# Kernel tuning notes

Hardware: AMD Instinct MI355X
Metric: run time of the kernel (lower is better)

## Reference

```python
import jax, jax.numpy as jnp
import numpy as np

NUM_HEADS = 32
NUM_KV_HEADS = 8
HEAD_DIM = 128
ROPE_THETA = 10000.0
HIDDEN = NUM_HEADS * HEAD_DIM


def setup_inputs() -> dict:
    key = jax.random.key(0)
    ks = jax.random.split(key, 5)
    B, S = 2, 2048
    hidden_states = jax.random.normal(ks[0], (B, S, HIDDEN), dtype=jnp.float32)
    wq = jax.random.normal(ks[1], (HIDDEN, HIDDEN), dtype=jnp.float32) * 0.02
    wk = jax.random.normal(ks[2], (NUM_KV_HEADS * HEAD_DIM, HIDDEN), dtype=jnp.float32) * 0.02
    wv = jax.random.normal(ks[3], (NUM_KV_HEADS * HEAD_DIM, HIDDEN), dtype=jnp.float32) * 0.02
    wo = jax.random.normal(ks[4], (HIDDEN, HIDDEN), dtype=jnp.float32) * 0.02
    position_ids = jnp.broadcast_to(jnp.arange(S, dtype=jnp.int64 if jax.config.read('jax_enable_x64') else jnp.int32)[None, :], (B, S))
    return {"hidden_states": hidden_states, "position_ids": position_ids,
            "wq": wq, "wk": wk, "wv": wv, "wo": wo}


def _rotate_half(x):
    x1, x2 = jnp.split(x, 2, axis=-1)
    return jnp.concatenate((-x2, x1), axis=-1)


def _rope_tables(position_ids, dtype):
    # inv_freq: [head_dim/2]
    inv_freq = 1.0 / (ROPE_THETA ** (jnp.arange(0, HEAD_DIM, 2, dtype=jnp.float32) / HEAD_DIM))
    # freqs per position: [B, S, head_dim/2] -> emb [B, S, head_dim]
    freqs = position_ids.astype(jnp.float32)[..., None] * inv_freq  # bsd2
    emb = jnp.concatenate((freqs, freqs), axis=-1)
    # unsqueeze head dim -> [B, 1, S, head_dim]
    return jnp.cos(emb).astype(dtype)[:, None], jnp.sin(emb).astype(dtype)[:, None]


def reference(hidden_states, position_ids, wq, wk, wv, wo):
    B, S, H = hidden_states.shape
    n_rep = NUM_HEADS // NUM_KV_HEADS
    # projections (torch Linear: x @ W^T)
    q = (hidden_states @ wq.T).reshape(B, S, NUM_HEADS, HEAD_DIM).transpose(0, 2, 1, 3)
    k = (hidden_states @ wk.T).reshape(B, S, NUM_KV_HEADS, HEAD_DIM).transpose(0, 2, 1, 3)
    v = (hidden_states @ wv.T).reshape(B, S, NUM_KV_HEADS, HEAD_DIM).transpose(0, 2, 1, 3)
    cos, sin = _rope_tables(position_ids, hidden_states.dtype)
    q = q * cos + _rotate_half(q) * sin
    k = k * cos + _rotate_half(k) * sin
    # repeat_kv: [B, kvH, S, D] -> [B, H, S, D]
    k = jnp.repeat(k, n_rep, axis=1)
    v = jnp.repeat(v, n_rep, axis=1)
    scale = 1.0 / jnp.sqrt(jnp.asarray(HEAD_DIM, dtype=hidden_states.dtype))
    scores = jnp.einsum('bhqd,bhkd->bhqk', q, k) * scale
    causal = jnp.tril(jnp.ones((S, S), dtype=bool))
    scores = jnp.where(causal[None, None], scores, jnp.finfo(scores.dtype).min)
    # softmax in fp32 then cast back (matches HF upcast)
    attn = jax.nn.softmax(scores.astype(jnp.float32), axis=-1).astype(q.dtype)
    out = jnp.einsum('bhqk,bhkd->bhqd', attn, v)
    out = out.transpose(0, 2, 1, 3).reshape(B, S, H)
    return out @ wo.T
```

## Files before the change

### kernel.cpp

```cpp
#include <hip/hip_runtime.h>
#include <stdint.h>

#define NH      32
#define NKVH    8
#define HD      128
#define BATCH   2
#define SEQ     2048
#define HIDDEN  4096
#define KVDIM   1024
#define TOKENS  (BATCH*SEQ)

typedef __bf16 bf16x8 __attribute__((ext_vector_type(8)));
typedef float  f32x4  __attribute__((ext_vector_type(4)));

__device__ __forceinline__ uint16_t f32_to_bf16(float f) {
  union { float f; uint32_t u; } v; v.f = f;
  uint32_t r = v.u + 0x7FFFu + ((v.u >> 16) & 1u);
  return (uint16_t)(r >> 16);
}
__device__ __forceinline__ float bf16_to_f32(uint16_t h) {
  union { uint32_t u; float f; } v; v.u = ((uint32_t)h) << 16;
  return v.f;
}
__device__ __forceinline__ bf16x8 ld_frag(const uint16_t* p) {
  return *(const bf16x8*)p;
}
#define MFMA_BF16(a,b,c) __builtin_amdgcn_mfma_f32_16x16x32_bf16((a),(b),(c),0,0,0)
#define NEG_BIG (-1.0e30f)

typedef __attribute__((address_space(1))) void as1_void;
typedef __attribute__((address_space(3))) void as3_void;
__device__ __forceinline__ void gload_lds16(const void* g, void* l) {
  __builtin_amdgcn_global_load_lds((as1_void*)g, (as3_void*)l, 16, 0, 0);
}

__device__ __forceinline__ void cvt8(const float* __restrict__ s,
                                     uint16_t* __restrict__ d, size_t i) {
  const float4* sp = (const float4*)s + 2*i;
  float4 a = sp[0], b = sp[1];
  union { uint16_t u[8]; uint4 v; } o;
  o.u[0]=f32_to_bf16(a.x); o.u[1]=f32_to_bf16(a.y);
  o.u[2]=f32_to_bf16(a.z); o.u[3]=f32_to_bf16(a.w);
  o.u[4]=f32_to_bf16(b.x); o.u[5]=f32_to_bf16(b.y);
  o.u[6]=f32_to_bf16(b.z); o.u[7]=f32_to_bf16(b.w);
  ((uint4*)d)[i] = o.v;
}

__global__ __launch_bounds__(256) void cvt_all(
    const float* __restrict__ X,  const float* __restrict__ Wq,
    const float* __restrict__ Wk, const float* __restrict__ Wv,
    uint16_t* __restrict__ R0, uint16_t* __restrict__ R1,
    uint16_t* __restrict__ R2, uint16_t* __restrict__ R3)
{
  int blk = blockIdx.x;
  const float* s; uint16_t* d; int b0;
  if (blk < 8192)       { s = X;  d = R0; b0 = 0; }
  else if (blk < 16384) { s = Wq; d = R1; b0 = 8192; }
  else if (blk < 18432) { s = Wk; d = R2; b0 = 16384; }
  else                  { s = Wv; d = R3; b0 = 18432; }
  cvt8(s, d, (size_t)(blk - b0)*256 + threadIdx.x);
}

__global__ __launch_bounds__(256) void cvt_one(
    const float* __restrict__ s, uint16_t* __restrict__ d)
{
  cvt8(s, d, (size_t)blockIdx.x*256 + threadIdx.x);
}

__device__ __forceinline__ void store_c(uint16_t* p, float v) { *p = f32_to_bf16(v); }
__device__ __forceinline__ void store_c(float*    p, float v) { *p = v; }

template <typename TC>
__device__ __forceinline__ void gemm_body(
    const uint16_t* __restrict__ A, const uint16_t* __restrict__ B,
    TC* __restrict__ C, int m0, int n0, int N, int K)
{
  __shared__ __align__(16) uint16_t As[3][128*32];
  __shared__ __align__(16) uint16_t Bs[3][128*32];
  const int tid  = threadIdx.x;
  const int wave = tid >> 6;
  const int lane = tid & 63;
  const int wm = (wave >> 1) * 64;
  const int wn = (wave & 1) * 64;
  const int srow = lane >> 2;
  const int scol = (((lane & 3) ^ ((lane >> 3) & 3)) * 8);
  const uint16_t* Ap = A + (size_t)(m0 + wave*16 + srow) * K + scol;
  const uint16_t* Bp = B + (size_t)(n0 + wave*16 + srow) * K + scol;
  const int wuo = wave*16*32;
  const int fr = lane & 15;
  const int fo = (((lane >> 4) ^ ((fr >> 1) & 3)) * 8);
  const int NT = K / 32;

  #pragma unroll
  for (int t = 0; t < 2; ++t) {
    gload_lds16(Ap + (size_t)t*32,                &As[t][wuo]);
    gload_lds16(Ap + (size_t)64*K + (size_t)t*32, &As[t][64*32 + wuo]);
    gload_lds16(Bp + (size_t)t*32,                &Bs[t][wuo]);
    gload_lds16(Bp + (size_t)64*K + (size_t)t*32, &Bs[t][64*32 + wuo]);
  }

  f32x4 acc[4][4] = {};
  int s_cur = 0, s_stage = 2;
  for (int t = 0; t < NT; ++t) {
    if (t < NT - 1) asm volatile("s_waitcnt vmcnt(4)" ::: "memory");
    else            asm volatile("s_waitcnt vmcnt(0)" ::: "memory");
    __builtin_amdgcn_s_barrier();
    asm volatile("" ::: "memory");

    if (t + 2 < NT) {
      const size_t k2 = (size_t)(t + 2) * 32;
      gload_lds16(Ap + k2,                &As[s_stage][wuo]);
      gload_lds16(Ap + (size_t)64*K + k2, &As[s_stage][64*32 + wuo]);
      gload_lds16(Bp + k2,                &Bs[s_stage][wuo]);
      gload_lds16(Bp + (size_t)64*K + k2, &Bs[s_stage][64*32 + wuo]);
    }

    const uint16_t* Asb = As[s_cur];
    const uint16_t* Bsb = Bs[s_cur];
    bf16x8 af[4], bfr[4];
    #pragma unroll
    for (int i = 0; i < 4; ++i) af[i]  = ld_frag(&Asb[(wm + i*16 + fr)*32 + fo]);
    #pragma unroll
    for (int j = 0; j < 4; ++j) bfr[j] = ld_frag(&Bsb[(wn + j*16 + fr)*32 + fo]);
    __builtin_amdgcn_s_setprio(1);
    #pragma unroll
    for (int i = 0; i < 4; ++i)
      #pragma unroll
      for (int j = 0; j < 4; ++j)
        acc[i][j] = MFMA_BF16(af[i], bfr[j], acc[i][j]);
    __builtin_amdgcn_s_setprio(0);

    s_cur   = (s_cur   == 2) ? 0 : s_cur + 1;
    s_stage = (s_stage == 2) ? 0 : s_stage + 1;
  }

  const int cr = (lane >> 4) * 4;
  const int cfr = lane & 15;
  #pragma unroll
  for (int i = 0; i < 4; ++i)
    #pragma unroll
    for (int j = 0; j < 4; ++j)
      #pragma unroll
      for (int r = 0; r < 4; ++r)
        store_c(&C[(size_t)(m0 + wm + i*16 + cr + r) * N + (n0 + wn + j*16 + cfr)],
                acc[i][j][r]);
}

__global__ __launch_bounds__(256, 3) void qkv_gemm(
    const uint16_t* __restrict__ X,
    const uint16_t* __restrict__ Wq, const uint16_t* __restrict__ Wk,
    const uint16_t* __restrict__ Wv,
    uint16_t* __restrict__ Qo, uint16_t* __restrict__ Ko, uint16_t* __restrict__ Vo)
{
  int bx = blockIdx.x;
  const uint16_t* B; uint16_t* C; int n0, N;
  if (bx < 32)      { B = Wq; C = Qo; n0 = bx*128;      N = HIDDEN; }
  else if (bx < 40) { B = Wk; C = Ko; n0 = (bx-32)*128; N = KVDIM;  }
  else              { B = Wv; C = Vo; n0 = (bx-40)*128; N = KVDIM;  }
  gemm_body<uint16_t>(X, B, C, blockIdx.y*128, n0, N, HIDDEN);
}

__global__ __launch_bounds__(256, 3) void out_gemm(
    const uint16_t* __restrict__ A, const uint16_t* __restrict__ B,
    float* __restrict__ C, int N, int K)
{
  gemm_body<float>(A, B, C, blockIdx.y*128, blockIdx.x*128, N, K);
}

__global__ __launch_bounds__(256) void rope_kernel(
    uint16_t* __restrict__ Q, uint16_t* __restrict__ K)
{
  int idx = blockIdx.x * 256 + threadIdx.x;
  int j = idx & 63;
  int rest = idx >> 6;
  int h = rest % (NH + NKVH);
  int t = rest / (NH + NKVH);
  float pos = (float)(t % SEQ);
  float inv_freq = __exp10f(-0.0625f * (float)j);
  float ang = pos * inv_freq;
  float s, c;
  __sincosf(ang, &s, &c);
  uint16_t* base = (h < NH) ? (Q + (size_t)t*HIDDEN + h*HD)
                            : (K + (size_t)t*KVDIM + (h-NH)*HD);
  float x1 = bf16_to_f32(base[j]);
  float x2 = bf16_to_f32(base[j+64]);
  base[j]    = f32_to_bf16(x1*c - x2*s);
  base[j+64] = f32_to_bf16(x2*c + x1*s);
}

__global__ __launch_bounds__(256) void transpose_v(
    const uint16_t* __restrict__ V, uint16_t* __restrict__ Vt)
{
  __shared__ uint16_t tile[64][66];
  int bh = blockIdx.z;  int b = bh >> 3, h = bh & 7;
  int s0 = blockIdx.x * 64;
  int d0 = blockIdx.y * 64;
  int tx = threadIdx.x & 63;
  int ty = threadIdx.x >> 6;
  const uint16_t* Vp = V + (size_t)b*SEQ*KVDIM + (size_t)h*HD;
  for (int r = ty; r < 64; r += 4)
    tile[r][tx] = Vp[(size_t)(s0 + r)*KVDIM + d0 + tx];
  __syncthreads();
  uint16_t* Vtp = Vt + ((size_t)b*NKVH + h)*HD*SEQ;
  for (int r = ty; r < 64; r += 4)
    Vtp[(size_t)(d0 + r)*SEQ + s0 + tx] = tile[tx][r];
}

#define KSTR 136
#define VSTR 72

__global__ __launch_bounds__(256, 4) void flash_attn(
    uint16_t* __restrict__ Q, const uint16_t* __restrict__ K,
    const uint16_t* __restrict__ Vt)
{
  __shared__ __align__(16) uint16_t Ks[64*KSTR];
  __shared__ __align__(16) uint16_t Vs[128*VSTR];
  uint16_t* Ps = Ks;

  const int tid  = threadIdx.x;
  const int wave = tid >> 6;
  const int lane = tid & 63;
  const int fr = lane & 15;
  const int g  = lane >> 4;
  const int fo = g * 8;
  const int bh = blockIdx.y;
  const int b = bh >> 5, h = bh & 31;
  const int kvh = h >> 2;

  uint16_t*       Qh = Q  + (size_t)b*SEQ*HIDDEN + (size_t)h*HD;
  const uint16_t* Kp = K  + (size_t)b*SEQ*KVDIM  + (size_t)kvh*HD;
  const uint16_t* Vp = Vt + ((size_t)b*NKVH + kvh)*HD*SEQ;

  #pragma unroll
  for (int pass = 0; pass < 2; ++pass) {
    const int qt = pass ? (31 - (int)blockIdx.x) : (int)blockIdx.x;
    const int q0 = qt * 64;
    const int qrow_base = q0 + wave*16 + g*4;

    bf16x8 qf[4];
    #pragma unroll
    for (int ks = 0; ks < 4; ++ks)
      qf[ks] = ld_frag(Qh + (size_t)(q0 + wave*16 + fr)*HIDDEN + ks*32 + fo);

    float m_i[4], l_i[4];
    f32x4 oacc[8] = {};
    #pragma unroll
    for (int r = 0; r < 4; ++r) { m_i[r] = NEG_BIG; l_i[r] = 0.f; }

    const int nkt = qt + 1;
    for (int kt = 0; kt < nkt; ++kt) {
      const int k0 = kt * 64;
      __syncthreads();
      #pragma unroll
      for (int i = 0; i < 4; ++i) {
        int gi = tid + i*256;
        int kr = gi >> 4, kc = (gi & 15) * 8;
        *(bf16x8*)&Ks[kr*KSTR + kc] = *(const bf16x8*)(Kp + (size_t)(k0 + kr)*KVDIM + kc);
        int vr = gi >> 3, vc = (gi & 7) * 8;
        *(bf16x8*)&Vs[vr*VSTR + vc] = *(const bf16x8*)(Vp + (size_t)vr*SEQ + k0 + vc);
      }
      __syncthreads();

      f32x4 sacc[4] = {};
      #pragma unroll
      for (int ks = 0; ks < 4; ++ks) {
        bf16x8 bk[4];
        #pragma unroll
        for (int j = 0; j < 4; ++j) bk[j] = ld_frag(&Ks[(j*16 + fr)*KSTR + ks*32 + fo]);
        #pragma unroll
        for (int j = 0; j < 4; ++j) sacc[j] = MFMA_BF16(qf[ks], bk[j], sacc[j]);
      }

      const bool diag = (kt == qt);
      #pragma unroll
      for (int r = 0; r < 4; ++r) {
        float vals[4];
        #pragma unroll
        for (int j = 0; j < 4; ++j) {
          float v = sacc[j][r] * 0.08838834764831845f;
          if (diag && (k0 + j*16 + fr > qrow_base + r)) v = NEG_BIG;
          vals[j] = v;
        }
        float mt = fmaxf(fmaxf(vals[0], vals[1]), fmaxf(vals[2], vals[3]));
        #pragma unroll
        for (int off = 1; off < 16; off <<= 1) mt = fmaxf(mt, __shfl_xor(mt, off, 64));
        float mn = fmaxf(m_i[r], mt);
        float alpha = __expf(fminf(m_i[r] - mn, 0.f));
        float lt = 0.f;
        #pragma unroll
        for (int j = 0; j < 4; ++j) {
          float p = __expf(fminf(vals[j] - mn, 0.f));
          sacc[j][r] = p;
          lt += p;
        }
        #pragma unroll
        for (int off = 1; off < 16; off <<= 1) lt += __shfl_xor(lt, off, 64);
        m_i[r] = mn;
        l_i[r] = l_i[r]*alpha + lt;
        #pragma unroll
        for (int n = 0; n < 8; ++n) oacc[n][r] *= alpha;
      }

      __syncthreads();

      #pragma unroll
      for (int j = 0; j < 4; ++j)
        #pragma unroll
        for (int r = 0; r < 4; ++r)
          Ps[(wave*16 + g*4 + r)*VSTR + j*16 + fr] = f32_to_bf16(sacc[j][r]);

      #pragma unroll
      for (int ks = 0; ks < 2; ++ks) {
        bf16x8 ap = ld_frag(&Ps[(wave*16 + fr)*VSTR + ks*32 + fo]);
        #pragma unroll
        for (int half = 0; half < 2; ++half) {
          bf16x8 bv[4];
          #pragma unroll
          for (int n = 0; n < 4; ++n)
            bv[n] = ld_frag(&Vs[((half*4 + n)*16 + fr)*VSTR + ks*32 + fo]);
          #pragma unroll
          for (int n = 0; n < 4; ++n)
            oacc[half*4 + n] = MFMA_BF16(ap, bv[n], oacc[half*4 + n]);
        }
      }
    }

    #pragma unroll
    for (int r = 0; r < 4; ++r) {
      float inv_l = 1.0f / l_i[r];
      #pragma unroll
      for (int n = 0; n < 8; ++n)
        Qh[(size_t)(qrow_base + r)*HIDDEN + n*16 + fr] = f32_to_bf16(oacc[n][r] * inv_l);
    }
    __syncthreads();
  }
}

extern "C" void kernel_launch(void* const* d_in, const int* in_sizes, int n_in,
                              void* d_out, int out_size, void* d_ws, size_t ws_size,
                              hipStream_t stream)
{
  (void)in_sizes; (void)n_in; (void)out_size; (void)ws_size;
  const float* hidden = (const float*)d_in[0];
  const float* wq = (const float*)d_in[2];
  const float* wk = (const float*)d_in[3];
  const float* wv = (const float*)d_in[4];
  const float* wo = (const float*)d_in[5];
  float* out = (float*)d_out;

  uint16_t* R0 = (uint16_t*)d_ws;
  uint16_t* R1 = R0 + (size_t)HIDDEN*HIDDEN;
  uint16_t* R2 = R1 + (size_t)HIDDEN*HIDDEN;
  uint16_t* R3 = R2 + (size_t)KVDIM*HIDDEN;
  uint16_t* Qb = R3 + (size_t)KVDIM*HIDDEN;
  uint16_t* Kb = Qb + (size_t)TOKENS*HIDDEN;
  uint16_t* Vb = Kb + (size_t)TOKENS*KVDIM;

  dim3 blk(256);
  cvt_all<<<dim3(20480), blk, 0, stream>>>(hidden, wq, wk, wv, R0, R1, R2, R3);
  qkv_gemm<<<dim3(48, TOKENS/128), blk, 0, stream>>>(R0, R1, R2, R3, Qb, Kb, Vb);
  rope_kernel<<<dim3(TOKENS*(NH+NKVH)*64/256), blk, 0, stream>>>(Qb, Kb);
  cvt_one<<<dim3(HIDDEN*HIDDEN/8/256), blk, 0, stream>>>(wo, R0);
  transpose_v<<<dim3(SEQ/64, HD/64, BATCH*NKVH), blk, 0, stream>>>(Vb, R1);
  flash_attn<<<dim3(16, BATCH*NH), blk, 0, stream>>>(Qb, Kb, R1);
  out_gemm<<<dim3(HIDDEN/128, TOKENS/128), blk, 0, stream>>>(Qb, R0, out, HIDDEN, HIDDEN);
}
```

Baseline: 840.5 us.

## Transpose QK^T MFMA layout and add lazy softmax rescaling

Swaps the MFMA operands so each lane holds a full query row's scores. This lets the row max and sum use two cross-lane shuffles instead of four per row, and the probabilities are written to LDS as packed 8-byte stores. It adds a lazy-rescale threshold that skips the alpha rescale of the output accumulator unless the max grows by more than 8, and sets s_setprio around the MFMA groups. The risk is a small loss of numerical margin, since exp values may reach about e^8 before rescaling, and the extra shuffles needed to map alpha and l back to the output layout.

```diff
diff --git a/kernel.cpp b/kernel.cpp
--- a/kernel.cpp
+++ b/kernel.cpp
@@ -235,17 +235,16 @@
   for (int pass = 0; pass < 2; ++pass) {
     const int qt = pass ? (31 - (int)blockIdx.x) : (int)blockIdx.x;
     const int q0 = qt * 64;
-    const int qrow_base = q0 + wave*16 + g*4;
+    const int qrow = q0 + wave*16 + fr;
+    const int orow_base = q0 + wave*16 + g*4;
 
     bf16x8 qf[4];
     #pragma unroll
     for (int ks = 0; ks < 4; ++ks)
       qf[ks] = ld_frag(Qh + (size_t)(q0 + wave*16 + fr)*HIDDEN + ks*32 + fo);
 
-    float m_i[4], l_i[4];
+    float m_i = NEG_BIG, l_i = 0.f;
     f32x4 oacc[8] = {};
-    #pragma unroll
-    for (int r = 0; r < 4; ++r) { m_i[r] = NEG_BIG; l_i[r] = 0.f; }
 
     const int nkt = qt + 1;
     for (int kt = 0; kt < nkt; ++kt) {
@@ -267,47 +266,67 @@
         bf16x8 bk[4];
         #pragma unroll
         for (int j = 0; j < 4; ++j) bk[j] = ld_frag(&Ks[(j*16 + fr)*KSTR + ks*32 + fo]);
-        #pragma unroll
-        for (int j = 0; j < 4; ++j) sacc[j] = MFMA_BF16(qf[ks], bk[j], sacc[j]);
+        __builtin_amdgcn_s_setprio(1);
+        #pragma unroll
+        for (int j = 0; j < 4; ++j) sacc[j] = MFMA_BF16(bk[j], qf[ks], sacc[j]);
+        __builtin_amdgcn_s_setprio(0);
       }
 
       const bool diag = (kt == qt);
       #pragma unroll
-      for (int r = 0; r < 4; ++r) {
-        float vals[4];
-        #pragma unroll
-        for (int j = 0; j < 4; ++j) {
+      for (int j = 0; j < 4; ++j)
+        #pragma unroll
+        for (int r = 0; r < 4; ++r) {
           float v = sacc[j][r] * 0.08838834764831845f;
-          if (diag && (k0 + j*16 + fr > qrow_base + r)) v = NEG_BIG;
-          vals[j] = v;
+          if (diag && (k0 + j*16 + g*4 + r > qrow)) v = NEG_BIG;
+          sacc[j][r] = v;
         }
-        float mt = fmaxf(fmaxf(vals[0], vals[1]), fmaxf(vals[2], vals[3]));
-        #pragma unroll
-        for (int off = 1; off < 16; off <<= 1) mt = fmaxf(mt, __shfl_xor(mt, off, 64));
-        float mn = fmaxf(m_i[r], mt);
-        float alpha = __expf(fminf(m_i[r] - mn, 0.f));
-        float lt = 0.f;
-        #pragma unroll
-        for (int j = 0; j < 4; ++j) {
-          float p = __expf(fminf(vals[j] - mn, 0.f));
-          sacc[j][r] = p;
-          lt += p;
+
+      float mt = sacc[0][0];
+      #pragma unroll
+      for (int j = 0; j < 4; ++j)
+        #pragma unroll
+        for (int r = 0; r < 4; ++r)
+          if (j | r) mt = fmaxf(mt, sacc[j][r]);
+      mt = fmaxf(mt, __shfl_xor(mt, 16, 64));
+      mt = fmaxf(mt, __shfl_xor(mt, 32, 64));
+
+      float alpha = 1.0f;
+      if (!__all(mt <= m_i + 8.0f)) {
+        float mn = fmaxf(m_i, mt);
+        alpha = __expf(m_i - mn);
+        m_i = mn;
+        #pragma unroll
+        for (int r = 0; r < 4; ++r) {
+          float ar = __shfl(alpha, g*4 + r, 64);
+          #pragma unroll
+          for (int n = 0; n < 8; ++n) oacc[n][r] *= ar;
         }
-        #pragma unroll
-        for (int off = 1; off < 16; off <<= 1) lt += __shfl_xor(lt, off, 64);
-        m_i[r] = mn;
-        l_i[r] = l_i[r]*alpha + lt;
-        #pragma unroll
-        for (int n = 0; n < 8; ++n) oacc[n][r] *= alpha;
-      }
+      }
+
+      float lt = 0.f;
+      uint2 pw[4];
+      #pragma unroll
+      for (int j = 0; j < 4; ++j) {
+        float p0 = __expf(sacc[j][0] - m_i);
+        float p1 = __expf(sacc[j][1] - m_i);
+        float p2 = __expf(sacc[j][2] - m_i);
+        float p3 = __expf(sacc[j][3] - m_i);
+        lt += (p0 + p1) + (p2 + p3);
+        union { uint16_t u[4]; uint2 v; } pk;
+        pk.u[0] = f32_to_bf16(p0); pk.u[1] = f32_to_bf16(p1);
+        pk.u[2] = f32_to_bf16(p2); pk.u[3] = f32_to_bf16(p3);
+        pw[j] = pk.v;
+      }
+      lt += __shfl_xor(lt, 16, 64);
+      lt += __shfl_xor(lt, 32, 64);
+      l_i = l_i * alpha + lt;
 
       __syncthreads();
 
       #pragma unroll
       for (int j = 0; j < 4; ++j)
-        #pragma unroll
-        for (int r = 0; r < 4; ++r)
-          Ps[(wave*16 + g*4 + r)*VSTR + j*16 + fr] = f32_to_bf16(sacc[j][r]);
+        *(uint2*)&Ps[(wave*16 + fr)*VSTR + j*16 + g*4] = pw[j];
 
       #pragma unroll
       for (int ks = 0; ks < 2; ++ks) {
@@ -318,19 +337,22 @@
           #pragma unroll
           for (int n = 0; n < 4; ++n)
             bv[n] = ld_frag(&Vs[((half*4 + n)*16 + fr)*VSTR + ks*32 + fo]);
+          __builtin_amdgcn_s_setprio(1);
           #pragma unroll
           for (int n = 0; n < 4; ++n)
             oacc[half*4 + n] = MFMA_BF16(ap, bv[n], oacc[half*4 + n]);
+          __builtin_amdgcn_s_setprio(0);
         }
       }
     }
 
     #pragma unroll
     for (int r = 0; r < 4; ++r) {
-      float inv_l = 1.0f / l_i[r];
+      float lr = __shfl(l_i, g*4 + r, 64);
+      float inv_l = 1.0f / lr;
       #pragma unroll
       for (int n = 0; n < 8; ++n)
-        Qh[(size_t)(qrow_base + r)*HIDDEN + n*16 + fr] = f32_to_bf16(oacc[n][r] * inv_l);
+        Qh[(size_t)(orow_base + r)*HIDDEN + n*16 + fr] = f32_to_bf16(oacc[n][r] * inv_l);
     }
     __syncthreads();
   }
```

New measurement: 802.0 us. -4.6%, faster.
